# Kernel optimization log

Hardware: AMD Instinct MI355X
Metric: run time of the kernel (lower is better)

## Reference

```python
import jax, jax.numpy as jnp
import numpy as np
from math import factorial, sqrt

RS_IN = [(64, 0, 0), (64, 1, 0), (32, 2, 0)]
BATCH = 256


def _w3j(j1, j2, j3, m1, m2, m3):
    # Racah formula for the Wigner 3j symbol (integer l's)
    if m1 + m2 + m3 != 0 or not (abs(j1 - j2) <= j3 <= j1 + j2):
        return 0.0
    if abs(m1) > j1 or abs(m2) > j2 or abs(m3) > j3:
        return 0.0
    f = factorial
    pref = (-1.0) ** (j1 - j2 - m3) * sqrt(
        f(j1 + j2 - j3) * f(j1 - j2 + j3) * f(-j1 + j2 + j3) / f(j1 + j2 + j3 + 1)
        * f(j1 + m1) * f(j1 - m1) * f(j2 + m2) * f(j2 - m2) * f(j3 + m3) * f(j3 - m3))
    kmin = max(0, j2 - j3 - m1, j1 - j3 + m2)
    kmax = min(j1 + j2 - j3, j1 - m1, j2 + m2)
    s = 0.0
    for k in range(kmin, kmax + 1):
        s += (-1.0) ** k / (f(k) * f(j1 + j2 - j3 - k) * f(j1 - m1 - k)
                            * f(j2 + m2 - k) * f(j3 - j2 + m1 + k) * f(j3 - j1 - m2 + k))
    return pref * s


def _q(l):
    # unitary change of basis: complex spherical harmonics -> real basis
    q = np.zeros((2 * l + 1, 2 * l + 1), dtype=complex)
    q[l, l] = 1.0
    for m in range(1, l + 1):
        q[l + m, l + m] = (-1) ** m / sqrt(2)
        q[l + m, l - m] = 1 / sqrt(2)
        q[l - m, l - m] = 1j / sqrt(2)
        q[l - m, l + m] = -1j * (-1) ** m / sqrt(2)
    return q


def _real_w3j(la, lb, lc):
    # real-basis Wigner 3j tensor of shape (2la+1, 2lb+1, 2lc+1), Frobenius norm 1
    Cc = np.zeros((2 * la + 1, 2 * lb + 1, 2 * lc + 1))
    for ma in range(-la, la + 1):
        for mb in range(-lb, lb + 1):
            mc = -(ma + mb)
            if abs(mc) <= lc:
                Cc[la + ma, lb + mb, lc + mc] = _w3j(la, lb, lc, ma, mb, mc)
    T = np.einsum('im,jn,ko,mno->ijk', _q(la), _q(lb), _q(lc), Cc.astype(complex))
    idx = np.argmax(np.abs(T))
    T = T / (T.flat[idx] / abs(T.flat[idx]))  # fix global phase -> real tensor
    assert np.abs(T.imag).max() < 1e-6
    return np.real(T)


def _simplify(Rs):
    out = []
    for mul, l, p in Rs:
        if out and out[-1][1:] == (l, p):
            out[-1] = (out[-1][0] + mul, l, p)
        elif mul > 0:
            out.append((mul, l, p))
    return out


def _build(Rs_in):
    # Replicates e3nn tensor_square(Rs_in, sorted=True) with 'component' normalization,
    # producing the sparse mixing matrix as (row, col_i, col_j, value) with
    # col = col_i * dim_in + col_j  (never materialized densely).
    Rs = _simplify(Rs_in)
    dim_in = sum(m * (2 * l + 1) for m, l, _ in Rs)
    rows, ci, cj, vals, Rs_out = [], [], [], [], []
    index_out = 0
    index_1 = 0
    for a, (mul1, l1, p1) in enumerate(Rs):
        dim1 = mul1 * (2 * l1 + 1)
        # diagonal block: irrep with itself (sym/antisym multiplicity pairs)
        for lo in range(0, 2 * l1 + 1):
            w_all = np.arange(mul1 * mul1)
            u, v = w_all // mul1, w_all % mul1
            mask = (u <= v) if lo % 2 == 0 else (u < v)
            u, v = u[mask], v[mask]
            cnt = u.size
            if cnt == 0:
                continue
            C = _real_w3j(lo, l1, l1) * sqrt(2 * lo + 1)  # component norm
            k, i1, i2 = np.nonzero(C)
            cv = C[k, i1, i2]
            w = np.arange(cnt)
            rows.append((w[:, None] * (2 * lo + 1) + k[None, :]).ravel() + index_out)
            ci.append((u[:, None] * (2 * l1 + 1) + i1[None, :]).ravel() + index_1)
            cj.append((v[:, None] * (2 * l1 + 1) + i2[None, :]).ravel() + index_1)
            vals.append(np.tile(cv, cnt))
            Rs_out.append((cnt, lo, p1 * p1))
            index_out += cnt * (2 * lo + 1)
        index_2 = index_1 + dim1
        # off-diagonal blocks
        for (mul2, l2, p2) in Rs[a + 1:]:
            dim2 = mul2 * (2 * l2 + 1)
            for lo in range(abs(l1 - l2), l1 + l2 + 1):
                C = _real_w3j(lo, l1, l2) * sqrt(2 * lo + 1)
                k, i1, i2 = np.nonzero(C)
                cv = C[k, i1, i2]
                cnt = mul1 * mul2
                w = np.arange(cnt)
                u, v = w // mul2, w % mul2
                rows.append((w[:, None] * (2 * lo + 1) + k[None, :]).ravel() + index_out)
                ci.append((u[:, None] * (2 * l1 + 1) + i1[None, :]).ravel() + index_1)
                cj.append((v[:, None] * (2 * l2 + 1) + i2[None, :]).ravel() + index_2)
                vals.append(np.tile(cv, cnt))
                Rs_out.append((cnt, lo, p1 * p2))
                index_out += cnt * (2 * lo + 1)
            index_2 += dim2
        index_1 += dim1
    Rs_out = _simplify(Rs_out)
    # stable sort of output irreps by (l, p) -> row permutation (sorted=True)
    xs, j = [], 0
    for mul, l, p in Rs_out:
        d = mul * (2 * l + 1)
        xs.append((l, p, mul, j, d))
        j += d
    old2new = np.empty(j, dtype=np.int64)
    i = 0
    for l, p, mul, jj, d in sorted(xs):
        old2new[jj:jj + d] = np.arange(i, i + d)
        i += d
    rows = old2new[np.concatenate(rows)]
    return (rows.astype(np.int32), np.concatenate(ci).astype(np.int32),
            np.concatenate(cj).astype(np.int32),
            np.concatenate(vals).astype(np.float32), int(i), int(dim_in))


_ROWS, _COLI, _COLJ, _VALS, _DIM_OUT, _DIM_IN = _build(RS_IN)


def setup_inputs() -> dict:
    key = jax.random.key(0)
    features = jax.random.normal(key, (BATCH, _DIM_IN), dtype=jnp.float32)
    return {
        'features': features,
        'vals': jnp.asarray(_VALS),
        'rows': jnp.asarray(_ROWS),
        'col_i': jnp.asarray(_COLI),
        'col_j': jnp.asarray(_COLJ),
        'dim_out': _DIM_OUT,
    }


def reference(features, vals, rows, col_i, col_j, dim_out):
    # out[z, r] = sum_e vals[e] * f[z, col_i[e]] * f[z, col_j[e]]  scattered into rows[e]
    f = features.reshape(-1, features.shape[-1])              # (Z, dim_in)
    contrib = vals[None, :] * f[:, col_i] * f[:, col_j]       # (Z, nnz)
    out = jax.ops.segment_sum(contrib.T, rows, num_segments=dim_out)  # (dim_out, Z)
    return out.T.reshape(*features.shape[:-1], -1)
```

## Files before the change

kernel.cpp:

```cpp
#include <hip/hip_runtime.h>

#define BATCH 256
#define ZTILE 16
#define PADF 20
#define CAP 16
#define DIN_CAP 416

__global__ __launch_bounds__(256) void prep(
    const float* __restrict__ f, const int* __restrict__ rows,
    int* __restrict__ rstart, int* __restrict__ rend,
    float* __restrict__ fT, int nnz, int dim_in, int nF, int do_transpose)
{
    const int i = blockIdx.x * blockDim.x + threadIdx.x;
    if (i < nnz) {
        const int r = rows[i];
        if (i == 0 || rows[i - 1] != r) rstart[r] = i;
        if (i == nnz - 1 || rows[i + 1] != r) rend[r] = i + 1;
    }
    if (do_transpose && i < nF) {
        const int z = i / dim_in;
        const int c = i - z * dim_in;
        fT[(size_t)c * BATCH + z] = f[i];
    }
}

__global__ __launch_bounds__(256) void tsq_main(
    const float* __restrict__ fT, const float* __restrict__ vals,
    const int* __restrict__ ci, const int* __restrict__ cj,
    const int* __restrict__ rstart, const int* __restrict__ rend,
    float* __restrict__ out, int dim_in, int dim_out, int nnz)
{
    __shared__ __align__(16) float fzT[DIN_CAP * PADF];

    const int r = blockIdx.x * blockDim.x + threadIdx.x;
    const bool valid = (r < dim_out);
    const int z0 = blockIdx.y * ZTILE;

    const int nchunk = dim_in * (ZTILE / 4);
    for (int i = threadIdx.x; i < nchunk; i += blockDim.x) {
        const int c  = i >> 2;
        const int zq = i & 3;
        const float4 v = *(const float4*)(fT + (size_t)c * BATCH + z0 + zq * 4);
        *(float4*)(fzT + c * PADF + zq * 4) = v;
    }

    int s = 0, e1 = 0;
    if (valid) {
        const int ss = rstart[r];
        const int ee = rend[r];
        if (ss >= 0 && ee >= ss && ee <= nnz) { s = ss; e1 = ee; }
    }
    const int cnt  = e1 - s;
    const int creg = cnt < CAP ? cnt : CAP;

    int pa_[CAP]; int pb_[CAP]; float ev_[CAP];
#pragma unroll
    for (int i = 0; i < CAP; ++i) {
        if (!__any(i < creg)) break;
        if (i < creg) {
            pa_[i] = ci[s + i] * (PADF * 4);
            pb_[i] = cj[s + i] * (PADF * 4);
            ev_[i] = vals[s + i];
        }
    }

    __syncthreads();

    float4 a0 = {0,0,0,0}, a1 = {0,0,0,0}, a2 = {0,0,0,0}, a3 = {0,0,0,0};
#pragma unroll
    for (int i = 0; i < CAP; ++i) {
        if (!__any(i < creg)) break;
        if (i < creg) {
            const float v = ev_[i];
            const char* ba = (const char*)fzT + pa_[i];
            const char* bb = (const char*)fzT + pb_[i];
            float4 xa, xb;
            xa = *(const float4*)(ba);      xb = *(const float4*)(bb);
            a0.x += v*xa.x*xb.x; a0.y += v*xa.y*xb.y; a0.z += v*xa.z*xb.z; a0.w += v*xa.w*xb.w;
            xa = *(const float4*)(ba + 16); xb = *(const float4*)(bb + 16);
            a1.x += v*xa.x*xb.x; a1.y += v*xa.y*xb.y; a1.z += v*xa.z*xb.z; a1.w += v*xa.w*xb.w;
            xa = *(const float4*)(ba + 32); xb = *(const float4*)(bb + 32);
            a2.x += v*xa.x*xb.x; a2.y += v*xa.y*xb.y; a2.z += v*xa.z*xb.z; a2.w += v*xa.w*xb.w;
            xa = *(const float4*)(ba + 48); xb = *(const float4*)(bb + 48);
            a3.x += v*xa.x*xb.x; a3.y += v*xa.y*xb.y; a3.z += v*xa.z*xb.z; a3.w += v*xa.w*xb.w;
        }
    }
    for (int e = s + CAP; e < e1; ++e) {
        const int a = ci[e], b = cj[e]; const float v = vals[e];
        const float* ba = fzT + a * PADF;
        const float* bb = fzT + b * PADF;
#pragma unroll
        for (int q = 0; q < 4; ++q) {
            const float4 xa = *(const float4*)(ba + q * 4);
            const float4 xb = *(const float4*)(bb + q * 4);
            float4* ac = q == 0 ? &a0 : q == 1 ? &a1 : q == 2 ? &a2 : &a3;
            ac->x += v*xa.x*xb.x; ac->y += v*xa.y*xb.y;
            ac->z += v*xa.z*xb.z; ac->w += v*xa.w*xb.w;
        }
    }

    if (valid) {
        float* o = out + (size_t)z0 * dim_out + r;
        const size_t d = dim_out;
        __builtin_nontemporal_store(a0.x, o);          __builtin_nontemporal_store(a0.y, o + d);
        __builtin_nontemporal_store(a0.z, o + 2*d);    __builtin_nontemporal_store(a0.w, o + 3*d);
        __builtin_nontemporal_store(a1.x, o + 4*d);    __builtin_nontemporal_store(a1.y, o + 5*d);
        __builtin_nontemporal_store(a1.z, o + 6*d);    __builtin_nontemporal_store(a1.w, o + 7*d);
        __builtin_nontemporal_store(a2.x, o + 8*d);    __builtin_nontemporal_store(a2.y, o + 9*d);
        __builtin_nontemporal_store(a2.z, o + 10*d);   __builtin_nontemporal_store(a2.w, o + 11*d);
        __builtin_nontemporal_store(a3.x, o + 12*d);   __builtin_nontemporal_store(a3.y, o + 13*d);
        __builtin_nontemporal_store(a3.z, o + 14*d);   __builtin_nontemporal_store(a3.w, o + 15*d);
    }
}

__global__ __launch_bounds__(256) void tsq_fallback(
    const float* __restrict__ f, const float* __restrict__ vals,
    const int* __restrict__ ci, const int* __restrict__ cj,
    const int* __restrict__ rstart, const int* __restrict__ rend,
    float* __restrict__ out, int dim_in, int dim_out, int nnz)
{
    const int r = blockIdx.x * blockDim.x + threadIdx.x;
    if (r >= dim_out) return;
    const int z = blockIdx.y;
    const float* __restrict__ fb = f + (size_t)z * dim_in;
    const int ss = rstart[r];
    const int ee = rend[r];
    float acc = 0.0f;
    if (ss >= 0 && ee >= ss && ee <= nnz) {
        for (int e = ss; e < ee; ++e)
            acc += vals[e] * fb[ci[e]] * fb[cj[e]];
    }
    out[(size_t)z * dim_out + r] = acc;
}

extern "C" void kernel_launch(void* const* d_in, const int* in_sizes, int n_in,
                              void* d_out, int out_size, void* d_ws, size_t ws_size,
                              hipStream_t stream)
{
    const float* f    = (const float*)d_in[0];
    const float* vals = (const float*)d_in[1];
    const int*   rows = (const int*)d_in[2];
    const int*   ci   = (const int*)d_in[3];
    const int*   cj   = (const int*)d_in[4];
    float*       out  = (float*)d_out;

    const int nnz     = in_sizes[1];
    const int nF      = in_sizes[0];
    const int dim_in  = nF / BATCH;
    const int dim_out = out_size / BATCH;

    int*   rstart = (int*)d_ws;
    int*   rend   = rstart + dim_out;
    float* fT     = (float*)(rend + dim_out);

    const int use_main = (dim_in <= DIN_CAP) &&
                         (ws_size >= (size_t)(2 * dim_out) * 4 + (size_t)nF * 4);

    const int prep_n = nnz > nF ? nnz : nF;
    prep<<<(prep_n + 255) / 256, 256, 0, stream>>>(f, rows, rstart, rend, fT,
                                                   nnz, dim_in, nF, use_main);

    if (use_main) {
        dim3 grid((dim_out + 255) / 256, BATCH / ZTILE);
        tsq_main<<<grid, 256, 0, stream>>>(fT, vals, ci, cj, rstart, rend, out,
                                           dim_in, dim_out, nnz);
    } else {
        dim3 grid((dim_out + 255) / 256, BATCH);
        tsq_fallback<<<grid, 256, 0, stream>>>(f, vals, ci, cj, rstart, rend,
                                               out, dim_in, dim_out, nnz);
    }
}
```

Baseline: 40.14 us.

## Loop over several smaller batch tiles per block, reusing row metadata

Each block now handles eight 8-sample batch tiles in sequence instead of one 16-sample tile. The per-row sparse indices and values are loaded into registers once and reused across all tiles, with the shared feature slice reloaded per tile behind barriers. The grid shrinks along the batch dimension, and a launch-bounds occupancy hint plus a smaller shared tile aim to raise waves per CU. The cost is fewer blocks, serialized tile loads with two barriers per tile, and no overlap between loading the next tile and computing the current one.

```diff
diff --git a/kernel.cpp b/kernel.cpp
--- a/kernel.cpp
+++ b/kernel.cpp
@@ -1,9 +1,10 @@
 #include <hip/hip_runtime.h>
 
 #define BATCH 256
-#define ZTILE 16
-#define PADF 20
-#define CAP 16
+#define ZTILE 8
+#define TPB 8
+#define PADF 12
+#define CAP 8
 #define DIN_CAP 416
 
 __global__ __launch_bounds__(256) void prep(
@@ -24,7 +25,7 @@
     }
 }
 
-__global__ __launch_bounds__(256) void tsq_main(
+__global__ __launch_bounds__(256, 8) void tsq_main(
     const float* __restrict__ fT, const float* __restrict__ vals,
     const int* __restrict__ ci, const int* __restrict__ cj,
     const int* __restrict__ rstart, const int* __restrict__ rend,
@@ -34,15 +35,6 @@
 
     const int r = blockIdx.x * blockDim.x + threadIdx.x;
     const bool valid = (r < dim_out);
-    const int z0 = blockIdx.y * ZTILE;
-
-    const int nchunk = dim_in * (ZTILE / 4);
-    for (int i = threadIdx.x; i < nchunk; i += blockDim.x) {
-        const int c  = i >> 2;
-        const int zq = i & 3;
-        const float4 v = *(const float4*)(fT + (size_t)c * BATCH + z0 + zq * 4);
-        *(float4*)(fzT + c * PADF + zq * 4) = v;
-    }
 
     int s = 0, e1 = 0;
     if (valid) {
@@ -64,52 +56,55 @@
         }
     }
 
-    __syncthreads();
+    const int zbase = blockIdx.y * (ZTILE * TPB);
+    const int nchunk = dim_in * (ZTILE / 4);
 
-    float4 a0 = {0,0,0,0}, a1 = {0,0,0,0}, a2 = {0,0,0,0}, a3 = {0,0,0,0};
+    for (int t = 0; t < TPB; ++t) {
+        const int z0 = zbase + t * ZTILE;
+
+        for (int i = threadIdx.x; i < nchunk; i += blockDim.x) {
+            const int c  = i >> 1;
+            const int zq = i & 1;
+            const float4 v = *(const float4*)(fT + (size_t)c * BATCH + z0 + zq * 4);
+            *(float4*)(fzT + c * PADF + zq * 4) = v;
+        }
+        __syncthreads();
+
+        float4 a0 = {0,0,0,0}, a1 = {0,0,0,0};
 #pragma unroll
-    for (int i = 0; i < CAP; ++i) {
-        if (!__any(i < creg)) break;
-        if (i < creg) {
-            const float v = ev_[i];
-            const char* ba = (const char*)fzT + pa_[i];
-            const char* bb = (const char*)fzT + pb_[i];
+        for (int i = 0; i < CAP; ++i) {
+            if (!__any(i < creg)) break;
+            if (i < creg) {
+                const float v = ev_[i];
+                const char* ba = (const char*)fzT + pa_[i];
+                const char* bb = (const char*)fzT + pb_[i];
+                float4 xa, xb;
+                xa = *(const float4*)(ba);      xb = *(const float4*)(bb);
+                a0.x += v*xa.x*xb.x; a0.y += v*xa.y*xb.y; a0.z += v*xa.z*xb.z; a0.w += v*xa.w*xb.w;
+                xa = *(const float4*)(ba + 16); xb = *(const float4*)(bb + 16);
+                a1.x += v*xa.x*xb.x; a1.y += v*xa.y*xb.y; a1.z += v*xa.z*xb.z; a1.w += v*xa.w*xb.w;
+            }
+        }
+        for (int e = s + CAP; e < e1; ++e) {
+            const int a = ci[e], b = cj[e]; const float v = vals[e];
+            const float* ba = fzT + a * PADF;
+            const float* bb = fzT + b * PADF;
             float4 xa, xb;
-            xa = *(const float4*)(ba);      xb = *(const float4*)(bb);
+            xa = *(const float4*)(ba);     xb = *(const float4*)(bb);
             a0.x += v*xa.x*xb.x; a0.y += v*xa.y*xb.y; a0.z += v*xa.z*xb.z; a0.w += v*xa.w*xb.w;
-            xa = *(const float4*)(ba + 16); xb = *(const float4*)(bb + 16);
+            xa = *(const float4*)(ba + 4); xb = *(const float4*)(bb + 4);
             a1.x += v*xa.x*xb.x; a1.y += v*xa.y*xb.y; a1.z += v*xa.z*xb.z; a1.w += v*xa.w*xb.w;
-            xa = *(const float4*)(ba + 32); xb = *(const float4*)(bb + 32);
-            a2.x += v*xa.x*xb.x; a2.y += v*xa.y*xb.y; a2.z += v*xa.z*xb.z; a2.w += v*xa.w*xb.w;
-            xa = *(const float4*)(ba + 48); xb = *(const float4*)(bb + 48);
-            a3.x += v*xa.x*xb.x; a3.y += v*xa.y*xb.y; a3.z += v*xa.z*xb.z; a3.w += v*xa.w*xb.w;
         }
-    }
-    for (int e = s + CAP; e < e1; ++e) {
-        const int a = ci[e], b = cj[e]; const float v = vals[e];
-        const float* ba = fzT + a * PADF;
-        const float* bb = fzT + b * PADF;
-#pragma unroll
-        for (int q = 0; q < 4; ++q) {
-            const float4 xa = *(const float4*)(ba + q * 4);
-            const float4 xb = *(const float4*)(bb + q * 4);
-            float4* ac = q == 0 ? &a0 : q == 1 ? &a1 : q == 2 ? &a2 : &a3;
-            ac->x += v*xa.x*xb.x; ac->y += v*xa.y*xb.y;
-            ac->z += v*xa.z*xb.z; ac->w += v*xa.w*xb.w;
+
+        if (valid) {
+            float* o = out + (size_t)z0 * dim_out + r;
+            const size_t d = dim_out;
+            __builtin_nontemporal_store(a0.x, o);        __builtin_nontemporal_store(a0.y, o + d);
+            __builtin_nontemporal_store(a0.z, o + 2*d);  __builtin_nontemporal_store(a0.w, o + 3*d);
+            __builtin_nontemporal_store(a1.x, o + 4*d);  __builtin_nontemporal_store(a1.y, o + 5*d);
+            __builtin_nontemporal_store(a1.z, o + 6*d);  __builtin_nontemporal_store(a1.w, o + 7*d);
         }
-    }
-
-    if (valid) {
-        float* o = out + (size_t)z0 * dim_out + r;
-        const size_t d = dim_out;
-        __builtin_nontemporal_store(a0.x, o);          __builtin_nontemporal_store(a0.y, o + d);
-        __builtin_nontemporal_store(a0.z, o + 2*d);    __builtin_nontemporal_store(a0.w, o + 3*d);
-        __builtin_nontemporal_store(a1.x, o + 4*d);    __builtin_nontemporal_store(a1.y, o + 5*d);
-        __builtin_nontemporal_store(a1.z, o + 6*d);    __builtin_nontemporal_store(a1.w, o + 7*d);
-        __builtin_nontemporal_store(a2.x, o + 8*d);    __builtin_nontemporal_store(a2.y, o + 9*d);
-        __builtin_nontemporal_store(a2.z, o + 10*d);   __builtin_nontemporal_store(a2.w, o + 11*d);
-        __builtin_nontemporal_store(a3.x, o + 12*d);   __builtin_nontemporal_store(a3.y, o + 13*d);
-        __builtin_nontemporal_store(a3.z, o + 14*d);   __builtin_nontemporal_store(a3.w, o + 15*d);
+        __syncthreads();
     }
 }
 
@@ -161,7 +156,7 @@
                                                    nnz, dim_in, nF, use_main);
 
     if (use_main) {
-        dim3 grid((dim_out + 255) / 256, BATCH / ZTILE);
+        dim3 grid((dim_out + 255) / 256, BATCH / (ZTILE * TPB));
         tsq_main<<<grid, 256, 0, stream>>>(fT, vals, ci, cj, rstart, rend, out,
                                            dim_in, dim_out, nnz);
     } else {
```

New measurement: 46.15 us. 1.15x slower.
